# Optimization experiments

Hardware: AMD Instinct MI355X
Metric: run time of the kernel (lower is better)

The kernel has to match this reference:

```python
import jax, jax.numpy as jnp
import numpy as np

V, H, B, T = 64, 128, 128, 512


def setup_inputs() -> dict:
    key = jax.random.key(0)
    ks = jax.random.split(key, 12)
    s = 0.05
    return {
        "x": jax.random.randint(ks[0], (B, T), 0, V),
        "emb": jax.random.normal(ks[1], (V, H), dtype=jnp.float32) * s,
        "w_ih_f": jax.random.normal(ks[2], (4 * H, H), dtype=jnp.float32) * s,
        "w_hh_f": jax.random.normal(ks[3], (4 * H, H), dtype=jnp.float32) * s,
        "b_ih_f": jax.random.normal(ks[4], (4 * H,), dtype=jnp.float32) * s,
        "b_hh_f": jax.random.normal(ks[5], (4 * H,), dtype=jnp.float32) * s,
        "w_ih_b": jax.random.normal(ks[6], (4 * H, H), dtype=jnp.float32) * s,
        "w_hh_b": jax.random.normal(ks[7], (4 * H, H), dtype=jnp.float32) * s,
        "b_ih_b": jax.random.normal(ks[8], (4 * H,), dtype=jnp.float32) * s,
        "b_hh_b": jax.random.normal(ks[9], (4 * H,), dtype=jnp.float32) * s,
        "fc_w": jax.random.normal(ks[10], (V, 2 * H), dtype=jnp.float32) * s,
        "fc_b": jax.random.normal(ks[11], (V,), dtype=jnp.float32) * s,
    }


def _lstm_scan(xp, w_hh):
    # xp: [T, B, 4H] precomputed input projections (+ biases); w_hh: [4H, H]
    h_dim = w_hh.shape[1]
    b = xp.shape[1]
    h0 = jnp.zeros((b, h_dim), dtype=xp.dtype)
    c0 = jnp.zeros((b, h_dim), dtype=xp.dtype)

    def step(carry, xt):
        h, c = carry
        gates = xt + h @ w_hh.T  # [B, 4H]
        i, f, g, o = jnp.split(gates, 4, axis=-1)  # torch gate order: i, f, g, o
        i = jax.nn.sigmoid(i)
        f = jax.nn.sigmoid(f)
        g = jnp.tanh(g)
        o = jax.nn.sigmoid(o)
        c = f * c + i * g
        h = o * jnp.tanh(c)
        return (h, c), h

    _, hs = jax.lax.scan(step, (h0, c0), xp)
    return hs  # [T, B, H]


def reference(x, emb, w_ih_f, w_hh_f, b_ih_f, b_hh_f,
              w_ih_b, w_hh_b, b_ih_b, b_hh_b, fc_w, fc_b):
    # embedding lookup: [B, T, H]
    e = emb[x]
    # precompute gate input projections for both directions
    xp_f = jnp.einsum('bth,gh->tbg', e, w_ih_f) + (b_ih_f + b_hh_f)  # [T,B,4H]
    xp_b = jnp.einsum('bth,gh->tbg', e, w_ih_b) + (b_ih_b + b_hh_b)
    h_f = _lstm_scan(xp_f, w_hh_f)                    # [T, B, H]
    h_b = _lstm_scan(xp_b[::-1], w_hh_b)[::-1]        # reversed-time dir, flipped back
    out = jnp.concatenate([h_f, h_b], axis=-1)        # [T, B, 2H]
    out = jnp.transpose(out, (1, 0, 2))               # [B, T, 2H]
    return out @ fc_w.T + fc_b                        # [B, T, V]
```

## Files before the change

kernel.cpp:

```cpp
#include <hip/hip_runtime.h>
#include <hip/hip_bf16.h>

#define B_ 128
#define T_ 512
#define H_ 128
#define V_ 64
#define G4_ 512

typedef _Float16 h2_t __attribute__((ext_vector_type(2)));
typedef _Float16 h8_t __attribute__((ext_vector_type(8)));
struct h8s { h2_t p[4]; };

__device__ __forceinline__ float dot2f(h2_t a, h2_t b, float c) {
#if __has_builtin(__builtin_amdgcn_fdot2)
  return __builtin_amdgcn_fdot2(a, b, c, false);
#else
  return fmaf((float)a[1], (float)b[1], fmaf((float)a[0], (float)b[0], c));
#endif
}

__device__ __forceinline__ float ex2(float x) {
#if __has_builtin(__builtin_amdgcn_exp2f)
  return __builtin_amdgcn_exp2f(x);
#else
  return exp2f(x);
#endif
}

__device__ __forceinline__ float rcpf_(float x) {
#if __has_builtin(__builtin_amdgcn_rcpf)
  return __builtin_amdgcn_rcpf(x);
#else
  return 1.0f / x;
#endif
}

#define QP_XOR1 0xB1
#define QP_XOR2 0x4E
#define QP_BC0 0x00
#define QP_BC1 0x55
#define QP_BC2 0xAA
#define QP_BC3 0xFF

template <int CTRL>
__device__ __forceinline__ float qperm(float v) {
#if __has_builtin(__builtin_amdgcn_update_dpp)
  return __builtin_bit_cast(
      float, __builtin_amdgcn_update_dpp(0, __builtin_bit_cast(int, v), CTRL,
                                         0xf, 0xf, true));
#else
  int lane = (int)(threadIdx.x & 3);
  int src;
  if constexpr (CTRL == QP_XOR1) src = lane ^ 1;
  else if constexpr (CTRL == QP_XOR2) src = lane ^ 2;
  else src = CTRL & 3;
  return __shfl(v, ((int)threadIdx.x & ~3) + src, 64);
#endif
}

__global__ __launch_bounds__(512) void k_tables(
    const float* __restrict__ emb,
    const float* __restrict__ w_ih_f, const float* __restrict__ b_ih_f,
    const float* __restrict__ b_hh_f,
    const float* __restrict__ w_ih_b, const float* __restrict__ b_ih_b,
    const float* __restrict__ b_hh_b,
    float* __restrict__ Ptab) {
  const int dir = blockIdx.x >> 6;
  const int v = blockIdx.x & 63;
  const int j = threadIdx.x;
  const float* w_ih = dir ? w_ih_b : w_ih_f;
  const float* bi = dir ? b_ih_b : b_ih_f;
  const float* bh = dir ? b_hh_b : b_hh_f;
  const float4* e4 = (const float4*)(emb + v * H_);
  const float4* w4 = (const float4*)(w_ih + j * H_);
  float a0 = 0.f, a1 = 0.f, a2 = 0.f, a3 = 0.f;
#pragma unroll
  for (int q = 0; q < H_ / 4; ++q) {
    float4 e = e4[q];
    float4 w = w4[q];
    a0 = fmaf(e.x, w.x, a0);
    a1 = fmaf(e.y, w.y, a1);
    a2 = fmaf(e.z, w.z, a2);
    a3 = fmaf(e.w, w.w, a3);
  }
  Ptab[dir * (V_ * G4_) + v * G4_ + j] = (a0 + a1) + (a2 + a3) + bi[j] + bh[j];
}

__global__ __launch_bounds__(512, 1) void k_scan(
    const int* __restrict__ x,
    const float* __restrict__ w_hh_f,
    const float* __restrict__ w_hh_b,
    const float* __restrict__ Ptab,
    _Float16* __restrict__ hs) {
  __shared__ __align__(16) float P[V_ * G4_];
  __shared__ int xoff[T_];
  __shared__ __align__(16) _Float16 hb[2][H_];

  const int tid = threadIdx.x;
  const int b = blockIdx.x >> 1;
  const int dir = blockIdx.x & 1;
  const int l = tid & 63;
  const int w = tid >> 6;
  const int g = l & 3;
  const int k = (w << 4) + (l >> 2);

  {
    const float4* src = (const float4*)(Ptab + dir * (V_ * G4_));
    float4* dst = (float4*)P;
#pragma unroll
    for (int i = 0; i < (V_ * G4_ / 4) / 512; ++i)
      dst[tid + i * 512] = src[tid + i * 512];
  }
  xoff[tid] = x[(b << 9) + tid] << 9;
  if (tid < H_) hb[0][tid] = (_Float16)0.f;

  const float* W = dir ? w_hh_b : w_hh_f;
  h2_t wr[4][16];
#pragma unroll
  for (int j = 0; j < 4; ++j) {
    const float2* wp = (const float2*)(W + (j * H_ + k) * H_ + g * 32);
#pragma unroll
    for (int e = 0; e < 16; ++e) {
      float2 ww = wp[e];
      wr[j][e] = h2_t{(_Float16)ww.x, (_Float16)ww.y};
    }
  }

  const float nm = (g == 2) ? -2.8853900817779268f : -1.4426950408889634f;
  const float sa = (g == 2) ? 2.f : 1.f;
  const float sb = (g == 2) ? -1.f : 0.f;

  float c0 = 0.f;
  _Float16* hsp = hs + ((size_t)(b << 9) << 8) + (dir << 7) + k;

  __syncthreads();

  int cur = 0;
  for (int s = 0; s < T_; ++s) {
    const int t = dir ? (T_ - 1 - s) : s;
    const h8_t* hq8 = (const h8_t*)(&hb[cur][g << 5]);
    h8s q0 = __builtin_bit_cast(h8s, hq8[0]);
    h8s q1 = __builtin_bit_cast(h8s, hq8[1]);
    h8s q2 = __builtin_bit_cast(h8s, hq8[2]);
    h8s q3 = __builtin_bit_cast(h8s, hq8[3]);
    float pv = P[xoff[t] + (g << 7) + k];

    float a0 = 0.f, a1 = 0.f, a2 = 0.f, a3 = 0.f;
#pragma unroll
    for (int e = 0; e < 4; ++e) {
      a0 = dot2f(q0.p[e], wr[0][e], a0);
      a1 = dot2f(q0.p[e], wr[1][e], a1);
      a2 = dot2f(q0.p[e], wr[2][e], a2);
      a3 = dot2f(q0.p[e], wr[3][e], a3);
    }
#pragma unroll
    for (int e = 0; e < 4; ++e) {
      a0 = dot2f(q1.p[e], wr[0][4 + e], a0);
      a1 = dot2f(q1.p[e], wr[1][4 + e], a1);
      a2 = dot2f(q1.p[e], wr[2][4 + e], a2);
      a3 = dot2f(q1.p[e], wr[3][4 + e], a3);
    }
#pragma unroll
    for (int e = 0; e < 4; ++e) {
      a0 = dot2f(q2.p[e], wr[0][8 + e], a0);
      a1 = dot2f(q2.p[e], wr[1][8 + e], a1);
      a2 = dot2f(q2.p[e], wr[2][8 + e], a2);
      a3 = dot2f(q2.p[e], wr[3][8 + e], a3);
    }
#pragma unroll
    for (int e = 0; e < 4; ++e) {
      a0 = dot2f(q3.p[e], wr[0][12 + e], a0);
      a1 = dot2f(q3.p[e], wr[1][12 + e], a1);
      a2 = dot2f(q3.p[e], wr[2][12 + e], a2);
      a3 = dot2f(q3.p[e], wr[3][12 + e], a3);
    }

    float s0 = a0 + qperm<QP_XOR1>(a0);
    float s1 = a1 + qperm<QP_XOR1>(a1);
    float s2 = a2 + qperm<QP_XOR1>(a2);
    float s3 = a3 + qperm<QP_XOR1>(a3);
    float A = (g & 1) ? s1 : s0;
    float Bv = (g & 1) ? s3 : s2;
    float A2 = A + qperm<QP_XOR2>(A);
    float B2 = Bv + qperm<QP_XOR2>(Bv);
    float gv = ((g & 2) ? B2 : A2) + pv;

    float e0 = ex2(nm * gv);
    float r0 = rcpf_(1.f + e0);
    float y = fmaf(sa, r0, sb);

    float yi = qperm<QP_BC0>(y);
    float yf = qperm<QP_BC1>(y);
    float yg = qperm<QP_BC2>(y);
    float yo = qperm<QP_BC3>(y);

    c0 = fmaf(yf, c0, yi * yg);
    float ec = ex2(-2.8853900817779268f * c0);
    float rc = rcpf_(1.f + ec);
    float tc = fmaf(2.f, rc, -1.f);
    float ht = yo * tc;

    if (g == 0) {
      _Float16 hh = (_Float16)ht;
      hb[cur ^ 1][k] = hh;
      hsp[(size_t)t << 8] = hh;
    }
    __syncthreads();
    cur ^= 1;
  }
}

__global__ __launch_bounds__(256) void k_fc(
    const _Float16* __restrict__ hs,
    const float* __restrict__ fc_w,
    const float* __restrict__ fc_b,
    float* __restrict__ out) {
  __shared__ __align__(16) _Float16 Wl[V_ * 2 * H_];
  __shared__ float bl[V_];
  const int tid = threadIdx.x;
  for (int i = tid; i < V_ * 2 * H_; i += 256) Wl[i] = (_Float16)fc_w[i];
  if (tid < V_) bl[tid] = fc_b[tid];
  __syncthreads();

  const size_t row = (size_t)blockIdx.x * 256 + tid;
  const h8_t* h8 = (const h8_t*)(hs + (row << 8));
  float acc[V_];
#pragma unroll
  for (int v = 0; v < V_; ++v) acc[v] = 0.f;

  for (int ch = 0; ch < 8; ++ch) {
    h8s hv0 = __builtin_bit_cast(h8s, h8[ch * 4 + 0]);
    h8s hv1 = __builtin_bit_cast(h8s, h8[ch * 4 + 1]);
    h8s hv2 = __builtin_bit_cast(h8s, h8[ch * 4 + 2]);
    h8s hv3 = __builtin_bit_cast(h8s, h8[ch * 4 + 3]);
#pragma unroll
    for (int v = 0; v < V_; ++v) {
      const h8_t* w8 = (const h8_t*)(Wl + v * 256 + ch * 32);
      float a = acc[v];
      h8s wv = __builtin_bit_cast(h8s, w8[0]);
      a = dot2f(hv0.p[0], wv.p[0], a);
      a = dot2f(hv0.p[1], wv.p[1], a);
      a = dot2f(hv0.p[2], wv.p[2], a);
      a = dot2f(hv0.p[3], wv.p[3], a);
      wv = __builtin_bit_cast(h8s, w8[1]);
      a = dot2f(hv1.p[0], wv.p[0], a);
      a = dot2f(hv1.p[1], wv.p[1], a);
      a = dot2f(hv1.p[2], wv.p[2], a);
      a = dot2f(hv1.p[3], wv.p[3], a);
      wv = __builtin_bit_cast(h8s, w8[2]);
      a = dot2f(hv2.p[0], wv.p[0], a);
      a = dot2f(hv2.p[1], wv.p[1], a);
      a = dot2f(hv2.p[2], wv.p[2], a);
      a = dot2f(hv2.p[3], wv.p[3], a);
      wv = __builtin_bit_cast(h8s, w8[3]);
      a = dot2f(hv3.p[0], wv.p[0], a);
      a = dot2f(hv3.p[1], wv.p[1], a);
      a = dot2f(hv3.p[2], wv.p[2], a);
      a = dot2f(hv3.p[3], wv.p[3], a);
      acc[v] = a;
    }
  }
  float* orow = out + (row << 6);
#pragma unroll
  for (int v = 0; v < V_; v += 4) {
    float4 o = make_float4(acc[v] + bl[v], acc[v + 1] + bl[v + 1],
                           acc[v + 2] + bl[v + 2], acc[v + 3] + bl[v + 3]);
    *(float4*)(orow + v) = o;
  }
}

extern "C" void kernel_launch(void* const* d_in, const int* in_sizes, int n_in,
                              void* d_out, int out_size, void* d_ws, size_t ws_size,
                              hipStream_t stream) {
  const int* x = (const int*)d_in[0];
  const float* emb = (const float*)d_in[1];
  const float* w_ih_f = (const float*)d_in[2];
  const float* w_hh_f = (const float*)d_in[3];
  const float* b_ih_f = (const float*)d_in[4];
  const float* b_hh_f = (const float*)d_in[5];
  const float* w_ih_b = (const float*)d_in[6];
  const float* w_hh_b = (const float*)d_in[7];
  const float* b_ih_b = (const float*)d_in[8];
  const float* b_hh_b = (const float*)d_in[9];
  const float* fc_w = (const float*)d_in[10];
  const float* fc_b = (const float*)d_in[11];
  float* out = (float*)d_out;

  float* Ptab = (float*)d_ws;
  _Float16* hs = (_Float16*)((char*)d_ws + (size_t)2 * V_ * G4_ * sizeof(float));

  k_tables<<<2 * V_, G4_, 0, stream>>>(emb, w_ih_f, b_ih_f, b_hh_f, w_ih_b,
                                       b_ih_b, b_hh_b, Ptab);
  k_scan<<<B_ * 2, G4_, 0, stream>>>(x, w_hh_f, w_hh_b, Ptab, hs);
  k_fc<<<B_ * T_ / 256, 256, 0, stream>>>(hs, fc_w, fc_b, out);
}
```

Baseline: 342.8 us.

## Process two batch sequences per scan block with batched hidden-state writes

Each scan block now runs the recurrence for two batch rows at once, halving the grid to 128 blocks and interleaving two independent dot-product and activation chains to hide latency. The input-projection table is re-laid out with gate index innermost so lookups are contiguous, and the next step's projection value is prefetched. Hidden states are staged in a 16-step shared-memory history and written out as 16-byte vector stores every 16 steps instead of scattered 2-byte stores. The cost is fewer blocks (128 on a 256-CU part) and a longer serial step per block, with extra register pressure.

```diff
diff --git a/kernel.cpp b/kernel.cpp
--- a/kernel.cpp
+++ b/kernel.cpp
@@ -83,7 +83,9 @@
     a2 = fmaf(e.z, w.z, a2);
     a3 = fmaf(e.w, w.w, a3);
   }
-  Ptab[dir * (V_ * G4_) + v * G4_ + j] = (a0 + a1) + (a2 + a3) + bi[j] + bh[j];
+  const int g = j >> 7, k = j & 127;
+  Ptab[dir * (V_ * G4_) + v * G4_ + (k << 2) + g] =
+      (a0 + a1) + (a2 + a3) + bi[j] + bh[j];
 }
 
 __global__ __launch_bounds__(512, 1) void k_scan(
@@ -93,16 +95,19 @@
     const float* __restrict__ Ptab,
     _Float16* __restrict__ hs) {
   __shared__ __align__(16) float P[V_ * G4_];
-  __shared__ int xoff[T_];
-  __shared__ __align__(16) _Float16 hb[2][H_];
+  __shared__ int xoff[2][T_];
+  __shared__ __align__(16) _Float16 hb[2][2][H_];
+  __shared__ __align__(16) _Float16 hist[2][16][H_];
 
   const int tid = threadIdx.x;
-  const int b = blockIdx.x >> 1;
-  const int dir = blockIdx.x & 1;
+  const int dir = blockIdx.x >> 6;
+  const int pr = blockIdx.x & 63;
+  const int b0 = pr << 1;
   const int l = tid & 63;
   const int w = tid >> 6;
   const int g = l & 3;
   const int k = (w << 4) + (l >> 2);
+  const int k4g = (k << 2) + g;
 
   {
     const float4* src = (const float4*)(Ptab + dir * (V_ * G4_));
@@ -111,8 +116,12 @@
     for (int i = 0; i < (V_ * G4_ / 4) / 512; ++i)
       dst[tid + i * 512] = src[tid + i * 512];
   }
-  xoff[tid] = x[(b << 9) + tid] << 9;
-  if (tid < H_) hb[0][tid] = (_Float16)0.f;
+  xoff[0][tid] = x[(b0 << 9) + tid] << 9;
+  xoff[1][tid] = x[((b0 + 1) << 9) + tid] << 9;
+  if (tid < H_) {
+    hb[0][0][tid] = (_Float16)0.f;
+    hb[1][0][tid] = (_Float16)0.f;
+  }
 
   const float* W = dir ? w_hh_b : w_hh_f;
   h2_t wr[4][16];
@@ -130,82 +139,140 @@
   const float sa = (g == 2) ? 2.f : 1.f;
   const float sb = (g == 2) ? -1.f : 0.f;
 
-  float c0 = 0.f;
-  _Float16* hsp = hs + ((size_t)(b << 9) << 8) + (dir << 7) + k;
+  float cA = 0.f, cB = 0.f;
 
   __syncthreads();
+
+  const int t0 = dir ? (T_ - 1) : 0;
+  float pvA = P[xoff[0][t0] + k4g];
+  float pvB = P[xoff[1][t0] + k4g];
 
   int cur = 0;
   for (int s = 0; s < T_; ++s) {
     const int t = dir ? (T_ - 1 - s) : s;
-    const h8_t* hq8 = (const h8_t*)(&hb[cur][g << 5]);
-    h8s q0 = __builtin_bit_cast(h8s, hq8[0]);
-    h8s q1 = __builtin_bit_cast(h8s, hq8[1]);
-    h8s q2 = __builtin_bit_cast(h8s, hq8[2]);
-    h8s q3 = __builtin_bit_cast(h8s, hq8[3]);
-    float pv = P[xoff[t] + (g << 7) + k];
-
-    float a0 = 0.f, a1 = 0.f, a2 = 0.f, a3 = 0.f;
+    const h8_t* hqA = (const h8_t*)(&hb[0][cur][g << 5]);
+    const h8_t* hqB = (const h8_t*)(&hb[1][cur][g << 5]);
+    h8s qA0 = __builtin_bit_cast(h8s, hqA[0]);
+    h8s qA1 = __builtin_bit_cast(h8s, hqA[1]);
+    h8s qA2 = __builtin_bit_cast(h8s, hqA[2]);
+    h8s qA3 = __builtin_bit_cast(h8s, hqA[3]);
+    h8s qB0 = __builtin_bit_cast(h8s, hqB[0]);
+    h8s qB1 = __builtin_bit_cast(h8s, hqB[1]);
+    h8s qB2 = __builtin_bit_cast(h8s, hqB[2]);
+    h8s qB3 = __builtin_bit_cast(h8s, hqB[3]);
+
+    const int sn = (s < T_ - 1) ? s + 1 : s;
+    const int tn = dir ? (T_ - 1 - sn) : sn;
+    const float pvnA = P[xoff[0][tn] + k4g];
+    const float pvnB = P[xoff[1][tn] + k4g];
+
+    float aA0 = 0.f, aA1 = 0.f, aA2 = 0.f, aA3 = 0.f;
+    float aB0 = 0.f, aB1 = 0.f, aB2 = 0.f, aB3 = 0.f;
 #pragma unroll
     for (int e = 0; e < 4; ++e) {
-      a0 = dot2f(q0.p[e], wr[0][e], a0);
-      a1 = dot2f(q0.p[e], wr[1][e], a1);
-      a2 = dot2f(q0.p[e], wr[2][e], a2);
-      a3 = dot2f(q0.p[e], wr[3][e], a3);
+      aA0 = dot2f(qA0.p[e], wr[0][e], aA0);
+      aA1 = dot2f(qA0.p[e], wr[1][e], aA1);
+      aA2 = dot2f(qA0.p[e], wr[2][e], aA2);
+      aA3 = dot2f(qA0.p[e], wr[3][e], aA3);
+      aB0 = dot2f(qB0.p[e], wr[0][e], aB0);
+      aB1 = dot2f(qB0.p[e], wr[1][e], aB1);
+      aB2 = dot2f(qB0.p[e], wr[2][e], aB2);
+      aB3 = dot2f(qB0.p[e], wr[3][e], aB3);
     }
 #pragma unroll
     for (int e = 0; e < 4; ++e) {
-      a0 = dot2f(q1.p[e], wr[0][4 + e], a0);
-      a1 = dot2f(q1.p[e], wr[1][4 + e], a1);
-      a2 = dot2f(q1.p[e], wr[2][4 + e], a2);
-      a3 = dot2f(q1.p[e], wr[3][4 + e], a3);
+      aA0 = dot2f(qA1.p[e], wr[0][4 + e], aA0);
+      aA1 = dot2f(qA1.p[e], wr[1][4 + e], aA1);
+      aA2 = dot2f(qA1.p[e], wr[2][4 + e], aA2);
+      aA3 = dot2f(qA1.p[e], wr[3][4 + e], aA3);
+      aB0 = dot2f(qB1.p[e], wr[0][4 + e], aB0);
+      aB1 = dot2f(qB1.p[e], wr[1][4 + e], aB1);
+      aB2 = dot2f(qB1.p[e], wr[2][4 + e], aB2);
+      aB3 = dot2f(qB1.p[e], wr[3][4 + e], aB3);
     }
 #pragma unroll
     for (int e = 0; e < 4; ++e) {
-      a0 = dot2f(q2.p[e], wr[0][8 + e], a0);
-      a1 = dot2f(q2.p[e], wr[1][8 + e], a1);
-      a2 = dot2f(q2.p[e], wr[2][8 + e], a2);
-      a3 = dot2f(q2.p[e], wr[3][8 + e], a3);
+      aA0 = dot2f(qA2.p[e], wr[0][8 + e], aA0);
+      aA1 = dot2f(qA2.p[e], wr[1][8 + e], aA1);
+      aA2 = dot2f(qA2.p[e], wr[2][8 + e], aA2);
+      aA3 = dot2f(qA2.p[e], wr[3][8 + e], aA3);
+      aB0 = dot2f(qB2.p[e], wr[0][8 + e], aB0);
+      aB1 = dot2f(qB2.p[e], wr[1][8 + e], aB1);
+      aB2 = dot2f(qB2.p[e], wr[2][8 + e], aB2);
+      aB3 = dot2f(qB2.p[e], wr[3][8 + e], aB3);
     }
 #pragma unroll
     for (int e = 0; e < 4; ++e) {
-      a0 = dot2f(q3.p[e], wr[0][12 + e], a0);
-      a1 = dot2f(q3.p[e], wr[1][12 + e], a1);
-      a2 = dot2f(q3.p[e], wr[2][12 + e], a2);
-      a3 = dot2f(q3.p[e], wr[3][12 + e], a3);
-    }
-
-    float s0 = a0 + qperm<QP_XOR1>(a0);
-    float s1 = a1 + qperm<QP_XOR1>(a1);
-    float s2 = a2 + qperm<QP_XOR1>(a2);
-    float s3 = a3 + qperm<QP_XOR1>(a3);
-    float A = (g & 1) ? s1 : s0;
-    float Bv = (g & 1) ? s3 : s2;
-    float A2 = A + qperm<QP_XOR2>(A);
-    float B2 = Bv + qperm<QP_XOR2>(Bv);
-    float gv = ((g & 2) ? B2 : A2) + pv;
-
-    float e0 = ex2(nm * gv);
-    float r0 = rcpf_(1.f + e0);
-    float y = fmaf(sa, r0, sb);
-
-    float yi = qperm<QP_BC0>(y);
-    float yf = qperm<QP_BC1>(y);
-    float yg = qperm<QP_BC2>(y);
-    float yo = qperm<QP_BC3>(y);
-
-    c0 = fmaf(yf, c0, yi * yg);
-    float ec = ex2(-2.8853900817779268f * c0);
-    float rc = rcpf_(1.f + ec);
-    float tc = fmaf(2.f, rc, -1.f);
-    float ht = yo * tc;
+      aA0 = dot2f(qA3.p[e], wr[0][12 + e], aA0);
+      aA1 = dot2f(qA3.p[e], wr[1][12 + e], aA1);
+      aA2 = dot2f(qA3.p[e], wr[2][12 + e], aA2);
+      aA3 = dot2f(qA3.p[e], wr[3][12 + e], aA3);
+      aB0 = dot2f(qB3.p[e], wr[0][12 + e], aB0);
+      aB1 = dot2f(qB3.p[e], wr[1][12 + e], aB1);
+      aB2 = dot2f(qB3.p[e], wr[2][12 + e], aB2);
+      aB3 = dot2f(qB3.p[e], wr[3][12 + e], aB3);
+    }
+
+    float sA0 = aA0 + qperm<QP_XOR1>(aA0);
+    float sA1 = aA1 + qperm<QP_XOR1>(aA1);
+    float sA2 = aA2 + qperm<QP_XOR1>(aA2);
+    float sA3 = aA3 + qperm<QP_XOR1>(aA3);
+    float sB0 = aB0 + qperm<QP_XOR1>(aB0);
+    float sB1 = aB1 + qperm<QP_XOR1>(aB1);
+    float sB2 = aB2 + qperm<QP_XOR1>(aB2);
+    float sB3 = aB3 + qperm<QP_XOR1>(aB3);
+    float AA = (g & 1) ? sA1 : sA0;
+    float BA = (g & 1) ? sA3 : sA2;
+    float AB = (g & 1) ? sB1 : sB0;
+    float BB = (g & 1) ? sB3 : sB2;
+    float A2A = AA + qperm<QP_XOR2>(AA);
+    float B2A = BA + qperm<QP_XOR2>(BA);
+    float A2B = AB + qperm<QP_XOR2>(AB);
+    float B2B = BB + qperm<QP_XOR2>(BB);
+    float gvA = ((g & 2) ? B2A : A2A) + pvA;
+    float gvB = ((g & 2) ? B2B : A2B) + pvB;
+
+    float yA = fmaf(sa, rcpf_(1.f + ex2(nm * gvA)), sb);
+    float yB = fmaf(sa, rcpf_(1.f + ex2(nm * gvB)), sb);
+
+    float yiA = qperm<QP_BC0>(yA);
+    float yfA = qperm<QP_BC1>(yA);
+    float ygA = qperm<QP_BC2>(yA);
+    float yoA = qperm<QP_BC3>(yA);
+    float yiB = qperm<QP_BC0>(yB);
+    float yfB = qperm<QP_BC1>(yB);
+    float ygB = qperm<QP_BC2>(yB);
+    float yoB = qperm<QP_BC3>(yB);
+
+    cA = fmaf(yfA, cA, yiA * ygA);
+    cB = fmaf(yfB, cB, yiB * ygB);
+    float tcA = fmaf(2.f, rcpf_(1.f + ex2(-2.8853900817779268f * cA)), -1.f);
+    float tcB = fmaf(2.f, rcpf_(1.f + ex2(-2.8853900817779268f * cB)), -1.f);
+    float htA = yoA * tcA;
+    float htB = yoB * tcB;
 
     if (g == 0) {
-      _Float16 hh = (_Float16)ht;
-      hb[cur ^ 1][k] = hh;
-      hsp[(size_t)t << 8] = hh;
+      _Float16 hA = (_Float16)htA;
+      _Float16 hB = (_Float16)htB;
+      hb[0][cur ^ 1][k] = hA;
+      hb[1][cur ^ 1][k] = hB;
+      hist[0][t & 15][k] = hA;
+      hist[1][t & 15][k] = hB;
+    }
+
+    if ((s & 15) == 15) {
+      __syncthreads();
+      const int base = t & ~15;
+      const int seq = tid >> 8;
+      const int rem = tid & 255;
+      const int tl = rem >> 4, q = rem & 15;
+      h8_t v8 = *(const h8_t*)(&hist[seq][tl][q << 3]);
+      *(h8_t*)(hs + (((size_t)((b0 + seq) << 9) + base + tl) << 8) +
+               (dir << 7) + (q << 3)) = v8;
     }
     __syncthreads();
+    pvA = pvnA;
+    pvB = pvnB;
     cur ^= 1;
   }
 }
@@ -291,6 +358,6 @@
 
   k_tables<<<2 * V_, G4_, 0, stream>>>(emb, w_ih_f, b_ih_f, b_hh_f, w_ih_b,
                                        b_ih_b, b_hh_b, Ptab);
-  k_scan<<<B_ * 2, G4_, 0, stream>>>(x, w_hh_f, w_hh_b, Ptab, hs);
+  k_scan<<<B_, 512, 0, stream>>>(x, w_hh_f, w_hh_b, Ptab, hs);
   k_fc<<<B_ * T_ / 256, 256, 0, stream>>>(hs, fc_w, fc_b, out);
 }
```

Result: slower. 546.0 us (+59.3%).

## Halve scan block to 256 threads with two hidden units per quad

Applied to the files above, without the earlier changes.

The recurrent scan kernel now runs 256 threads per block, and each 4-lane quad computes two hidden units. That doubles the register-held fp16 weights per thread and the dot products per lane. The shared-memory copy of the projection table is dropped: Ptab is re-laid out so each lane reads its two gate inputs as one float2 from global memory, prefetched one step ahead. Hidden-state stores go into a 16-step shared history buffer and are flushed as vectorized 16-byte writes, replacing per-step scalar stores. The aim is cheaper block-wide barriers and less setup and store traffic, at the cost of more serial work per lane and higher register pressure.

```diff
diff --git a/kernel.cpp b/kernel.cpp
--- a/kernel.cpp
+++ b/kernel.cpp
@@ -67,12 +67,12 @@
     float* __restrict__ Ptab) {
   const int dir = blockIdx.x >> 6;
   const int v = blockIdx.x & 63;
-  const int j = threadIdx.x;
+  const int j0 = threadIdx.x;
   const float* w_ih = dir ? w_ih_b : w_ih_f;
   const float* bi = dir ? b_ih_b : b_ih_f;
   const float* bh = dir ? b_hh_b : b_hh_f;
   const float4* e4 = (const float4*)(emb + v * H_);
-  const float4* w4 = (const float4*)(w_ih + j * H_);
+  const float4* w4 = (const float4*)(w_ih + j0 * H_);
   float a0 = 0.f, a1 = 0.f, a2 = 0.f, a3 = 0.f;
 #pragma unroll
   for (int q = 0; q < H_ / 4; ++q) {
@@ -83,129 +83,176 @@
     a2 = fmaf(e.z, w.z, a2);
     a3 = fmaf(e.w, w.w, a3);
   }
-  Ptab[dir * (V_ * G4_) + v * G4_ + j] = (a0 + a1) + (a2 + a3) + bi[j] + bh[j];
-}
-
-__global__ __launch_bounds__(512, 1) void k_scan(
+  const int g = j0 >> 7, k = j0 & 127;
+  const int Q = k & 63, jj = k >> 6;
+  Ptab[dir * (V_ * G4_) + v * G4_ + (Q << 3) + (g << 1) + jj] =
+      (a0 + a1) + (a2 + a3) + bi[j0] + bh[j0];
+}
+
+__global__ __launch_bounds__(256, 1) void k_scan(
     const int* __restrict__ x,
     const float* __restrict__ w_hh_f,
     const float* __restrict__ w_hh_b,
     const float* __restrict__ Ptab,
     _Float16* __restrict__ hs) {
-  __shared__ __align__(16) float P[V_ * G4_];
   __shared__ int xoff[T_];
   __shared__ __align__(16) _Float16 hb[2][H_];
+  __shared__ __align__(16) _Float16 hist[16][H_];
 
   const int tid = threadIdx.x;
   const int b = blockIdx.x >> 1;
   const int dir = blockIdx.x & 1;
-  const int l = tid & 63;
-  const int w = tid >> 6;
-  const int g = l & 3;
-  const int k = (w << 4) + (l >> 2);
-
-  {
-    const float4* src = (const float4*)(Ptab + dir * (V_ * G4_));
-    float4* dst = (float4*)P;
-#pragma unroll
-    for (int i = 0; i < (V_ * G4_ / 4) / 512; ++i)
-      dst[tid + i * 512] = src[tid + i * 512];
-  }
+  const int Q = tid >> 2;
+  const int q = tid & 3;
+
   xoff[tid] = x[(b << 9) + tid] << 9;
+  xoff[256 + tid] = x[(b << 9) + 256 + tid] << 9;
   if (tid < H_) hb[0][tid] = (_Float16)0.f;
 
   const float* W = dir ? w_hh_b : w_hh_f;
-  h2_t wr[4][16];
-#pragma unroll
-  for (int j = 0; j < 4; ++j) {
-    const float2* wp = (const float2*)(W + (j * H_ + k) * H_ + g * 32);
-#pragma unroll
-    for (int e = 0; e < 16; ++e) {
-      float2 ww = wp[e];
-      wr[j][e] = h2_t{(_Float16)ww.x, (_Float16)ww.y};
-    }
-  }
-
-  const float nm = (g == 2) ? -2.8853900817779268f : -1.4426950408889634f;
-  const float sa = (g == 2) ? 2.f : 1.f;
-  const float sb = (g == 2) ? -1.f : 0.f;
-
-  float c0 = 0.f;
-  _Float16* hsp = hs + ((size_t)(b << 9) << 8) + (dir << 7) + k;
+  h2_t wr[4][2][16];
+#pragma unroll
+  for (int g = 0; g < 4; ++g)
+#pragma unroll
+    for (int jj = 0; jj < 2; ++jj) {
+      const float2* wp =
+          (const float2*)(W + (g * H_ + Q + 64 * jj) * H_ + q * 32);
+#pragma unroll
+      for (int e = 0; e < 16; ++e) {
+        float2 ww = wp[e];
+        wr[g][jj][e] = h2_t{(_Float16)ww.x, (_Float16)ww.y};
+      }
+    }
+
+  const float nm = (q == 2) ? -2.8853900817779268f : -1.4426950408889634f;
+  const float sa = (q == 2) ? 2.f : 1.f;
+  const float sb = (q == 2) ? -1.f : 0.f;
+
+  float c0 = 0.f, c1 = 0.f;
+
+  const float* Pg = Ptab + dir * (V_ * G4_) + (Q << 3) + (q << 1);
 
   __syncthreads();
+
+  const int t0 = dir ? (T_ - 1) : 0;
+  float2 pv = *(const float2*)(Pg + xoff[t0]);
 
   int cur = 0;
   for (int s = 0; s < T_; ++s) {
     const int t = dir ? (T_ - 1 - s) : s;
-    const h8_t* hq8 = (const h8_t*)(&hb[cur][g << 5]);
-    h8s q0 = __builtin_bit_cast(h8s, hq8[0]);
-    h8s q1 = __builtin_bit_cast(h8s, hq8[1]);
-    h8s q2 = __builtin_bit_cast(h8s, hq8[2]);
-    h8s q3 = __builtin_bit_cast(h8s, hq8[3]);
-    float pv = P[xoff[t] + (g << 7) + k];
-
-    float a0 = 0.f, a1 = 0.f, a2 = 0.f, a3 = 0.f;
+    const h8_t* hq8 = (const h8_t*)(&hb[cur][q << 5]);
+    h8s h0 = __builtin_bit_cast(h8s, hq8[0]);
+    h8s h1 = __builtin_bit_cast(h8s, hq8[1]);
+    h8s h2v = __builtin_bit_cast(h8s, hq8[2]);
+    h8s h3 = __builtin_bit_cast(h8s, hq8[3]);
+
+    const int sn = (s < T_ - 1) ? s + 1 : s;
+    const int tn = dir ? (T_ - 1 - sn) : sn;
+    const float2 pvn = *(const float2*)(Pg + xoff[tn]);
+
+    float a00 = 0.f, a01 = 0.f, a10 = 0.f, a11 = 0.f;
+    float a20 = 0.f, a21 = 0.f, a30 = 0.f, a31 = 0.f;
 #pragma unroll
     for (int e = 0; e < 4; ++e) {
-      a0 = dot2f(q0.p[e], wr[0][e], a0);
-      a1 = dot2f(q0.p[e], wr[1][e], a1);
-      a2 = dot2f(q0.p[e], wr[2][e], a2);
-      a3 = dot2f(q0.p[e], wr[3][e], a3);
+      a00 = dot2f(h0.p[e], wr[0][0][e], a00);
+      a01 = dot2f(h0.p[e], wr[0][1][e], a01);
+      a10 = dot2f(h0.p[e], wr[1][0][e], a10);
+      a11 = dot2f(h0.p[e], wr[1][1][e], a11);
+      a20 = dot2f(h0.p[e], wr[2][0][e], a20);
+      a21 = dot2f(h0.p[e], wr[2][1][e], a21);
+      a30 = dot2f(h0.p[e], wr[3][0][e], a30);
+      a31 = dot2f(h0.p[e], wr[3][1][e], a31);
     }
 #pragma unroll
     for (int e = 0; e < 4; ++e) {
-      a0 = dot2f(q1.p[e], wr[0][4 + e], a0);
-      a1 = dot2f(q1.p[e], wr[1][4 + e], a1);
-      a2 = dot2f(q1.p[e], wr[2][4 + e], a2);
-      a3 = dot2f(q1.p[e], wr[3][4 + e], a3);
+      a00 = dot2f(h1.p[e], wr[0][0][4 + e], a00);
+      a01 = dot2f(h1.p[e], wr[0][1][4 + e], a01);
+      a10 = dot2f(h1.p[e], wr[1][0][4 + e], a10);
+      a11 = dot2f(h1.p[e], wr[1][1][4 + e], a11);
+      a20 = dot2f(h1.p[e], wr[2][0][4 + e], a20);
+      a21 = dot2f(h1.p[e], wr[2][1][4 + e], a21);
+      a30 = dot2f(h1.p[e], wr[3][0][4 + e], a30);
+      a31 = dot2f(h1.p[e], wr[3][1][4 + e], a31);
     }
 #pragma unroll
     for (int e = 0; e < 4; ++e) {
-      a0 = dot2f(q2.p[e], wr[0][8 + e], a0);
-      a1 = dot2f(q2.p[e], wr[1][8 + e], a1);
-      a2 = dot2f(q2.p[e], wr[2][8 + e], a2);
-      a3 = dot2f(q2.p[e], wr[3][8 + e], a3);
+      a00 = dot2f(h2v.p[e], wr[0][0][8 + e], a00);
+      a01 = dot2f(h2v.p[e], wr[0][1][8 + e], a01);
+      a10 = dot2f(h2v.p[e], wr[1][0][8 + e], a10);
+      a11 = dot2f(h2v.p[e], wr[1][1][8 + e], a11);
+      a20 = dot2f(h2v.p[e], wr[2][0][8 + e], a20);
+      a21 = dot2f(h2v.p[e], wr[2][1][8 + e], a21);
+      a30 = dot2f(h2v.p[e], wr[3][0][8 + e], a30);
+      a31 = dot2f(h2v.p[e], wr[3][1][8 + e], a31);
     }
 #pragma unroll
     for (int e = 0; e < 4; ++e) {
-      a0 = dot2f(q3.p[e], wr[0][12 + e], a0);
-      a1 = dot2f(q3.p[e], wr[1][12 + e], a1);
-      a2 = dot2f(q3.p[e], wr[2][12 + e], a2);
-      a3 = dot2f(q3.p[e], wr[3][12 + e], a3);
-    }
-
-    float s0 = a0 + qperm<QP_XOR1>(a0);
-    float s1 = a1 + qperm<QP_XOR1>(a1);
-    float s2 = a2 + qperm<QP_XOR1>(a2);
-    float s3 = a3 + qperm<QP_XOR1>(a3);
-    float A = (g & 1) ? s1 : s0;
-    float Bv = (g & 1) ? s3 : s2;
-    float A2 = A + qperm<QP_XOR2>(A);
-    float B2 = Bv + qperm<QP_XOR2>(Bv);
-    float gv = ((g & 2) ? B2 : A2) + pv;
-
-    float e0 = ex2(nm * gv);
-    float r0 = rcpf_(1.f + e0);
-    float y = fmaf(sa, r0, sb);
-
-    float yi = qperm<QP_BC0>(y);
-    float yf = qperm<QP_BC1>(y);
-    float yg = qperm<QP_BC2>(y);
-    float yo = qperm<QP_BC3>(y);
-
-    c0 = fmaf(yf, c0, yi * yg);
-    float ec = ex2(-2.8853900817779268f * c0);
-    float rc = rcpf_(1.f + ec);
-    float tc = fmaf(2.f, rc, -1.f);
-    float ht = yo * tc;
-
-    if (g == 0) {
-      _Float16 hh = (_Float16)ht;
-      hb[cur ^ 1][k] = hh;
-      hsp[(size_t)t << 8] = hh;
+      a00 = dot2f(h3.p[e], wr[0][0][12 + e], a00);
+      a01 = dot2f(h3.p[e], wr[0][1][12 + e], a01);
+      a10 = dot2f(h3.p[e], wr[1][0][12 + e], a10);
+      a11 = dot2f(h3.p[e], wr[1][1][12 + e], a11);
+      a20 = dot2f(h3.p[e], wr[2][0][12 + e], a20);
+      a21 = dot2f(h3.p[e], wr[2][1][12 + e], a21);
+      a30 = dot2f(h3.p[e], wr[3][0][12 + e], a30);
+      a31 = dot2f(h3.p[e], wr[3][1][12 + e], a31);
+    }
+
+    float s00 = a00 + qperm<QP_XOR1>(a00);
+    float s10 = a10 + qperm<QP_XOR1>(a10);
+    float s20 = a20 + qperm<QP_XOR1>(a20);
+    float s30 = a30 + qperm<QP_XOR1>(a30);
+    float s01 = a01 + qperm<QP_XOR1>(a01);
+    float s11 = a11 + qperm<QP_XOR1>(a11);
+    float s21 = a21 + qperm<QP_XOR1>(a21);
+    float s31 = a31 + qperm<QP_XOR1>(a31);
+    float mA0 = (q & 1) ? s10 : s00;
+    float mB0 = (q & 1) ? s30 : s20;
+    float mA1 = (q & 1) ? s11 : s01;
+    float mB1 = (q & 1) ? s31 : s21;
+    float uA0 = mA0 + qperm<QP_XOR2>(mA0);
+    float uB0 = mB0 + qperm<QP_XOR2>(mB0);
+    float uA1 = mA1 + qperm<QP_XOR2>(mA1);
+    float uB1 = mB1 + qperm<QP_XOR2>(mB1);
+    float gv0 = ((q & 2) ? uB0 : uA0) + pv.x;
+    float gv1 = ((q & 2) ? uB1 : uA1) + pv.y;
+
+    float y0 = fmaf(sa, rcpf_(1.f + ex2(nm * gv0)), sb);
+    float y1 = fmaf(sa, rcpf_(1.f + ex2(nm * gv1)), sb);
+
+    float yi0 = qperm<QP_BC0>(y0);
+    float yf0 = qperm<QP_BC1>(y0);
+    float yg0 = qperm<QP_BC2>(y0);
+    float yo0 = qperm<QP_BC3>(y0);
+    float yi1 = qperm<QP_BC0>(y1);
+    float yf1 = qperm<QP_BC1>(y1);
+    float yg1 = qperm<QP_BC2>(y1);
+    float yo1 = qperm<QP_BC3>(y1);
+
+    c0 = fmaf(yf0, c0, yi0 * yg0);
+    c1 = fmaf(yf1, c1, yi1 * yg1);
+    float tc0 = fmaf(2.f, rcpf_(1.f + ex2(-2.8853900817779268f * c0)), -1.f);
+    float tc1 = fmaf(2.f, rcpf_(1.f + ex2(-2.8853900817779268f * c1)), -1.f);
+    float ht0 = yo0 * tc0;
+    float ht1 = yo1 * tc1;
+
+    if (q == 0) {
+      _Float16 h0w = (_Float16)ht0;
+      _Float16 h1w = (_Float16)ht1;
+      hb[cur ^ 1][Q] = h0w;
+      hb[cur ^ 1][Q + 64] = h1w;
+      hist[t & 15][Q] = h0w;
+      hist[t & 15][Q + 64] = h1w;
     }
     __syncthreads();
+
+    if ((s & 15) == 15) {
+      const int base = t & ~15;
+      const int tl = tid >> 4, ch = tid & 15;
+      h8_t v8 = *(const h8_t*)(&hist[tl][ch << 3]);
+      *(h8_t*)(hs + (((size_t)((b << 9) + base + tl)) << 8) + (dir << 7) +
+               (ch << 3)) = v8;
+    }
+    pv = pvn;
     cur ^= 1;
   }
 }
@@ -291,6 +338,6 @@
 
   k_tables<<<2 * V_, G4_, 0, stream>>>(emb, w_ih_f, b_ih_f, b_hh_f, w_ih_b,
                                        b_ih_b, b_hh_b, Ptab);
-  k_scan<<<B_ * 2, G4_, 0, stream>>>(x, w_hh_f, w_hh_b, Ptab, hs);
+  k_scan<<<B_ * 2, 256, 0, stream>>>(x, w_hh_f, w_hh_b, Ptab, hs);
   k_fc<<<B_ * T_ / 256, 256, 0, stream>>>(hs, fc_w, fc_b, out);
 }
```

Result: slower. 372.9 us (+8.8%).

## Batch 16 sequences per block and run LSTM recurrence on MFMA

Applied to the files above, without the earlier changes.

Each scan block now handles 16 batch rows for one direction and computes the recurrent matmul with 16x16x32 f16 MFMA instructions instead of per-lane fdot2, so the grid drops from 256 blocks to 16. The gate table is re-laid out so MFMA accumulators can be seeded directly from it, and the next step's table values are prefetched. Hidden states are kept in a swizzled 16-step shared history and flushed to global every 8 steps in time-major order, and the FC kernel's output indexing is changed to match. The aim is to cut per-step instruction and sync cost. The trade-off is that only 16 CUs are used, so most of the GPU sits idle.

```diff
diff --git a/kernel.cpp b/kernel.cpp
--- a/kernel.cpp
+++ b/kernel.cpp
@@ -7,6 +7,8 @@
 #define V_ 64
 #define G4_ 512
 
+typedef _Float16 f16x8 __attribute__((ext_vector_type(8)));
+typedef float f32x4 __attribute__((ext_vector_type(4)));
 typedef _Float16 h2_t __attribute__((ext_vector_type(2)));
 typedef _Float16 h8_t __attribute__((ext_vector_type(8)));
 struct h8s { h2_t p[4]; };
@@ -35,27 +37,11 @@
 #endif
 }
 
-#define QP_XOR1 0xB1
-#define QP_XOR2 0x4E
-#define QP_BC0 0x00
-#define QP_BC1 0x55
-#define QP_BC2 0xAA
-#define QP_BC3 0xFF
-
-template <int CTRL>
-__device__ __forceinline__ float qperm(float v) {
-#if __has_builtin(__builtin_amdgcn_update_dpp)
-  return __builtin_bit_cast(
-      float, __builtin_amdgcn_update_dpp(0, __builtin_bit_cast(int, v), CTRL,
-                                         0xf, 0xf, true));
-#else
-  int lane = (int)(threadIdx.x & 3);
-  int src;
-  if constexpr (CTRL == QP_XOR1) src = lane ^ 1;
-  else if constexpr (CTRL == QP_XOR2) src = lane ^ 2;
-  else src = CTRL & 3;
-  return __shfl(v, ((int)threadIdx.x & ~3) + src, 64);
-#endif
+__device__ __forceinline__ float sigm(float x) {
+  return rcpf_(1.f + ex2(-1.4426950408889634f * x));
+}
+__device__ __forceinline__ float th(float x) {
+  return fmaf(2.f, rcpf_(1.f + ex2(-2.8853900817779268f * x)), -1.f);
 }
 
 __global__ __launch_bounds__(512) void k_tables(
@@ -67,12 +53,12 @@
     float* __restrict__ Ptab) {
   const int dir = blockIdx.x >> 6;
   const int v = blockIdx.x & 63;
-  const int j = threadIdx.x;
+  const int j0 = threadIdx.x;
   const float* w_ih = dir ? w_ih_b : w_ih_f;
   const float* bi = dir ? b_ih_b : b_ih_f;
   const float* bh = dir ? b_hh_b : b_hh_f;
   const float4* e4 = (const float4*)(emb + v * H_);
-  const float4* w4 = (const float4*)(w_ih + j * H_);
+  const float4* w4 = (const float4*)(w_ih + j0 * H_);
   float a0 = 0.f, a1 = 0.f, a2 = 0.f, a3 = 0.f;
 #pragma unroll
   for (int q = 0; q < H_ / 4; ++q) {
@@ -83,130 +69,167 @@
     a2 = fmaf(e.z, w.z, a2);
     a3 = fmaf(e.w, w.w, a3);
   }
-  Ptab[dir * (V_ * G4_) + v * G4_ + j] = (a0 + a1) + (a2 + a3) + bi[j] + bh[j];
-}
-
-__global__ __launch_bounds__(512, 1) void k_scan(
+  const int g = j0 >> 7, k = j0 & 127;
+  Ptab[dir * (V_ * G4_) + v * G4_ + ((k >> 4) << 6) + ((k & 15) << 2) + g] =
+      (a0 + a1) + (a2 + a3) + bi[j0] + bh[j0];
+}
+
+__global__ __launch_bounds__(512, 2) void k_scan(
     const int* __restrict__ x,
     const float* __restrict__ w_hh_f,
     const float* __restrict__ w_hh_b,
     const float* __restrict__ Ptab,
     _Float16* __restrict__ hs) {
-  __shared__ __align__(16) float P[V_ * G4_];
-  __shared__ int xoff[T_];
-  __shared__ __align__(16) _Float16 hb[2][H_];
+  __shared__ __align__(16) _Float16 hist[2][8][16 * H_];
+  __shared__ int xoff[T_ * 16];
 
   const int tid = threadIdx.x;
-  const int b = blockIdx.x >> 1;
-  const int dir = blockIdx.x & 1;
-  const int l = tid & 63;
-  const int w = tid >> 6;
-  const int g = l & 3;
-  const int k = (w << 4) + (l >> 2);
+  const int w = tid >> 6, l = tid & 63, cc = l & 15, grp = l >> 4;
+  const int dir = blockIdx.x & 1, bg = blockIdx.x >> 1;
+
+#pragma unroll
+  for (int bb = 0; bb < 16; ++bb)
+    xoff[tid * 16 + bb] = x[((bg * 16 + bb) << 9) + tid] << 11;
+
+  const float* W = dir ? w_hh_b : w_hh_f;
+  f16x8 Bf[4][4];
+#pragma unroll
+  for (int tau = 0; tau < 4; ++tau)
+#pragma unroll
+    for (int kt = 0; kt < 4; ++kt) {
+      const int j = tau * H_ + w * 16 + cc;
+      const int kb = kt * 32 + grp * 8;
+      float4 u0 = *(const float4*)(W + j * H_ + kb);
+      float4 u1 = *(const float4*)(W + j * H_ + kb + 4);
+      Bf[tau][kt] = f16x8{(_Float16)u0.x, (_Float16)u0.y, (_Float16)u0.z,
+                          (_Float16)u0.w, (_Float16)u1.x, (_Float16)u1.y,
+                          (_Float16)u1.z, (_Float16)u1.w};
+    }
 
   {
-    const float4* src = (const float4*)(Ptab + dir * (V_ * G4_));
-    float4* dst = (float4*)P;
-#pragma unroll
-    for (int i = 0; i < (V_ * G4_ / 4) / 512; ++i)
-      dst[tid + i * 512] = src[tid + i * 512];
-  }
-  xoff[tid] = x[(b << 9) + tid] << 9;
-  if (tid < H_) hb[0][tid] = (_Float16)0.f;
-
-  const float* W = dir ? w_hh_b : w_hh_f;
-  h2_t wr[4][16];
-#pragma unroll
-  for (int j = 0; j < 4; ++j) {
-    const float2* wp = (const float2*)(W + (j * H_ + k) * H_ + g * 32);
-#pragma unroll
-    for (int e = 0; e < 16; ++e) {
-      float2 ww = wp[e];
-      wr[j][e] = h2_t{(_Float16)ww.x, (_Float16)ww.y};
-    }
-  }
-
-  const float nm = (g == 2) ? -2.8853900817779268f : -1.4426950408889634f;
-  const float sa = (g == 2) ? 2.f : 1.f;
-  const float sb = (g == 2) ? -1.f : 0.f;
-
-  float c0 = 0.f;
-  _Float16* hsp = hs + ((size_t)(b << 9) << 8) + (dir << 7) + k;
-
+    unsigned* hz = (unsigned*)&hist[1][7][0];
+    hz[tid] = 0;
+    hz[tid + 512] = 0;
+  }
+
+  float c0 = 0.f, c1 = 0.f, c2 = 0.f, c3 = 0.f;
   __syncthreads();
 
-  int cur = 0;
+  const int swa = (cc & 7) << 4;
+  int aoff[4];
+#pragma unroll
+  for (int kt = 0; kt < 4; ++kt)
+    aoff[kt] = cc * 256 + ((kt * 64 + grp * 16) ^ swa);
+
+  int woff[4];
+#pragma unroll
+  for (int r = 0; r < 4; ++r) {
+    const int b = grp * 4 + r;
+    woff[r] = b * 256 + ((w * 32 + cc * 2) ^ ((b & 7) << 4));
+  }
+
+  const char* Pb =
+      (const char*)(Ptab + (size_t)dir * (V_ * G4_) + w * 64 + cc * 4);
+
+  f32x4 pA, pB, pC, pD;
+  {
+    const int t0 = dir ? (T_ - 1) : 0;
+    int4 xv = *(const int4*)&xoff[t0 * 16 + grp * 4];
+    float4 q0 = *(const float4*)(Pb + xv.x);
+    float4 q1 = *(const float4*)(Pb + xv.y);
+    float4 q2 = *(const float4*)(Pb + xv.z);
+    float4 q3 = *(const float4*)(Pb + xv.w);
+    pA = f32x4{q0.x, q1.x, q2.x, q3.x};
+    pB = f32x4{q0.y, q1.y, q2.y, q3.y};
+    pC = f32x4{q0.z, q1.z, q2.z, q3.z};
+    pD = f32x4{q0.w, q1.w, q2.w, q3.w};
+  }
+
   for (int s = 0; s < T_; ++s) {
-    const int t = dir ? (T_ - 1 - s) : s;
-    const h8_t* hq8 = (const h8_t*)(&hb[cur][g << 5]);
-    h8s q0 = __builtin_bit_cast(h8s, hq8[0]);
-    h8s q1 = __builtin_bit_cast(h8s, hq8[1]);
-    h8s q2 = __builtin_bit_cast(h8s, hq8[2]);
-    h8s q3 = __builtin_bit_cast(h8s, hq8[3]);
-    float pv = P[xoff[t] + (g << 7) + k];
-
-    float a0 = 0.f, a1 = 0.f, a2 = 0.f, a3 = 0.f;
-#pragma unroll
-    for (int e = 0; e < 4; ++e) {
-      a0 = dot2f(q0.p[e], wr[0][e], a0);
-      a1 = dot2f(q0.p[e], wr[1][e], a1);
-      a2 = dot2f(q0.p[e], wr[2][e], a2);
-      a3 = dot2f(q0.p[e], wr[3][e], a3);
-    }
-#pragma unroll
-    for (int e = 0; e < 4; ++e) {
-      a0 = dot2f(q1.p[e], wr[0][4 + e], a0);
-      a1 = dot2f(q1.p[e], wr[1][4 + e], a1);
-      a2 = dot2f(q1.p[e], wr[2][4 + e], a2);
-      a3 = dot2f(q1.p[e], wr[3][4 + e], a3);
-    }
-#pragma unroll
-    for (int e = 0; e < 4; ++e) {
-      a0 = dot2f(q2.p[e], wr[0][8 + e], a0);
-      a1 = dot2f(q2.p[e], wr[1][8 + e], a1);
-      a2 = dot2f(q2.p[e], wr[2][8 + e], a2);
-      a3 = dot2f(q2.p[e], wr[3][8 + e], a3);
-    }
-#pragma unroll
-    for (int e = 0; e < 4; ++e) {
-      a0 = dot2f(q3.p[e], wr[0][12 + e], a0);
-      a1 = dot2f(q3.p[e], wr[1][12 + e], a1);
-      a2 = dot2f(q3.p[e], wr[2][12 + e], a2);
-      a3 = dot2f(q3.p[e], wr[3][12 + e], a3);
-    }
-
-    float s0 = a0 + qperm<QP_XOR1>(a0);
-    float s1 = a1 + qperm<QP_XOR1>(a1);
-    float s2 = a2 + qperm<QP_XOR1>(a2);
-    float s3 = a3 + qperm<QP_XOR1>(a3);
-    float A = (g & 1) ? s1 : s0;
-    float Bv = (g & 1) ? s3 : s2;
-    float A2 = A + qperm<QP_XOR2>(A);
-    float B2 = Bv + qperm<QP_XOR2>(Bv);
-    float gv = ((g & 2) ? B2 : A2) + pv;
-
-    float e0 = ex2(nm * gv);
-    float r0 = rcpf_(1.f + e0);
-    float y = fmaf(sa, r0, sb);
-
-    float yi = qperm<QP_BC0>(y);
-    float yf = qperm<QP_BC1>(y);
-    float yg = qperm<QP_BC2>(y);
-    float yo = qperm<QP_BC3>(y);
-
-    c0 = fmaf(yf, c0, yi * yg);
-    float ec = ex2(-2.8853900817779268f * c0);
-    float rc = rcpf_(1.f + ec);
-    float tc = fmaf(2.f, rc, -1.f);
-    float ht = yo * tc;
-
-    if (g == 0) {
-      _Float16 hh = (_Float16)ht;
-      hb[cur ^ 1][k] = hh;
-      hsp[(size_t)t << 8] = hh;
-    }
+    const int pm = (s + 15) & 15;
+    const char* hsrc = (const char*)&hist[pm >> 3][pm & 7][0];
+    f16x8 A0 = *(const f16x8*)(hsrc + aoff[0]);
+    f16x8 A1 = *(const f16x8*)(hsrc + aoff[1]);
+    f16x8 A2 = *(const f16x8*)(hsrc + aoff[2]);
+    f16x8 A3 = *(const f16x8*)(hsrc + aoff[3]);
+
+    const int sn = (s < T_ - 1) ? s + 1 : s;
+    const int tn = dir ? (T_ - 1 - sn) : sn;
+    int4 xv = *(const int4*)&xoff[tn * 16 + grp * 4];
+    float4 q0 = *(const float4*)(Pb + xv.x);
+    float4 q1 = *(const float4*)(Pb + xv.y);
+    float4 q2 = *(const float4*)(Pb + xv.z);
+    float4 q3 = *(const float4*)(Pb + xv.w);
+
+    f32x4 a0 = pA, a1 = pB, a2 = pC, a3 = pD;
+    a0 = __builtin_amdgcn_mfma_f32_16x16x32_f16(A0, Bf[0][0], a0, 0, 0, 0);
+    a1 = __builtin_amdgcn_mfma_f32_16x16x32_f16(A0, Bf[1][0], a1, 0, 0, 0);
+    a2 = __builtin_amdgcn_mfma_f32_16x16x32_f16(A0, Bf[2][0], a2, 0, 0, 0);
+    a3 = __builtin_amdgcn_mfma_f32_16x16x32_f16(A0, Bf[3][0], a3, 0, 0, 0);
+    a0 = __builtin_amdgcn_mfma_f32_16x16x32_f16(A1, Bf[0][1], a0, 0, 0, 0);
+    a1 = __builtin_amdgcn_mfma_f32_16x16x32_f16(A1, Bf[1][1], a1, 0, 0, 0);
+    a2 = __builtin_amdgcn_mfma_f32_16x16x32_f16(A1, Bf[2][1], a2, 0, 0, 0);
+    a3 = __builtin_amdgcn_mfma_f32_16x16x32_f16(A1, Bf[3][1], a3, 0, 0, 0);
+    a0 = __builtin_amdgcn_mfma_f32_16x16x32_f16(A2, Bf[0][2], a0, 0, 0, 0);
+    a1 = __builtin_amdgcn_mfma_f32_16x16x32_f16(A2, Bf[1][2], a1, 0, 0, 0);
+    a2 = __builtin_amdgcn_mfma_f32_16x16x32_f16(A2, Bf[2][2], a2, 0, 0, 0);
+    a3 = __builtin_amdgcn_mfma_f32_16x16x32_f16(A2, Bf[3][2], a3, 0, 0, 0);
+    a0 = __builtin_amdgcn_mfma_f32_16x16x32_f16(A3, Bf[0][3], a0, 0, 0, 0);
+    a1 = __builtin_amdgcn_mfma_f32_16x16x32_f16(A3, Bf[1][3], a1, 0, 0, 0);
+    a2 = __builtin_amdgcn_mfma_f32_16x16x32_f16(A3, Bf[2][3], a2, 0, 0, 0);
+    a3 = __builtin_amdgcn_mfma_f32_16x16x32_f16(A3, Bf[3][3], a3, 0, 0, 0);
+
+    float hv0, hv1, hv2, hv3;
+    {
+      float yi = sigm(a0[0]), yf = sigm(a1[0]), yg = th(a2[0]), yo = sigm(a3[0]);
+      c0 = fmaf(yf, c0, yi * yg);
+      hv0 = yo * th(c0);
+    }
+    {
+      float yi = sigm(a0[1]), yf = sigm(a1[1]), yg = th(a2[1]), yo = sigm(a3[1]);
+      c1 = fmaf(yf, c1, yi * yg);
+      hv1 = yo * th(c1);
+    }
+    {
+      float yi = sigm(a0[2]), yf = sigm(a1[2]), yg = th(a2[2]), yo = sigm(a3[2]);
+      c2 = fmaf(yf, c2, yi * yg);
+      hv2 = yo * th(c2);
+    }
+    {
+      float yi = sigm(a0[3]), yf = sigm(a1[3]), yg = th(a2[3]), yo = sigm(a3[3]);
+      c3 = fmaf(yf, c3, yi * yg);
+      hv3 = yo * th(c3);
+    }
+
+    const int pc = s & 15;
+    char* hdst = (char*)&hist[pc >> 3][pc & 7][0];
+    *(_Float16*)(hdst + woff[0]) = (_Float16)hv0;
+    *(_Float16*)(hdst + woff[1]) = (_Float16)hv1;
+    *(_Float16*)(hdst + woff[2]) = (_Float16)hv2;
+    *(_Float16*)(hdst + woff[3]) = (_Float16)hv3;
+
+    pA = f32x4{q0.x, q1.x, q2.x, q3.x};
+    pB = f32x4{q0.y, q1.y, q2.y, q3.y};
+    pC = f32x4{q0.z, q1.z, q2.z, q3.z};
+    pD = f32x4{q0.w, q1.w, q2.w, q3.w};
+
     __syncthreads();
-    cur ^= 1;
+
+    if ((s & 7) == 7) {
+      const int ph = (s >> 3) & 1;
+      const int sb = s - 7;
+#pragma unroll
+      for (int i = 0; i < 4; ++i) {
+        const int chunk = tid + i * 512;
+        const int kc = chunk & 15, b = (chunk >> 4) & 15, tl = (chunk >> 8) & 7;
+        const int tb = dir ? (T_ - 1 - (sb + tl)) : (sb + tl);
+        f16x8 vv = *(const f16x8*)((const char*)&hist[ph][tl][0] + b * 256 +
+                                   ((kc * 16) ^ ((b & 7) << 4)));
+        *(f16x8*)((unsigned short*)hs +
+                  (((size_t)tb * B_ + bg * 16 + b) << 8) + (dir << 7) +
+                  (kc << 3)) = vv;
+      }
+    }
   }
 }
 
@@ -260,7 +283,8 @@
       acc[v] = a;
     }
   }
-  float* orow = out + (row << 6);
+  const int t = (int)(row >> 7), gb = (int)(row & 127);
+  float* orow = out + (((size_t)gb << 9) + t) * V_;
 #pragma unroll
   for (int v = 0; v < V_; v += 4) {
     float4 o = make_float4(acc[v] + bl[v], acc[v + 1] + bl[v + 1],
@@ -291,6 +315,6 @@
 
   k_tables<<<2 * V_, G4_, 0, stream>>>(emb, w_ih_f, b_ih_f, b_hh_f, w_ih_b,
                                        b_ih_b, b_hh_b, Ptab);
-  k_scan<<<B_ * 2, G4_, 0, stream>>>(x, w_hh_f, w_hh_b, Ptab, hs);
+  k_scan<<<16, 512, 0, stream>>>(x, w_hh_f, w_hh_b, Ptab, hs);
   k_fc<<<B_ * T_ / 256, 256, 0, stream>>>(hs, fc_w, fc_b, out);
 }
```

New measurement: 537.9 us. +56.9%, slower.
